# Kernel tuning notes

Measured on AMD Instinct MI355X. Metric: run time of the kernel, lower is better.

The kernel has to match this reference:

```python
import jax, jax.numpy as jnp
import numpy as np

D_MODEL = 1024
NUM_HEADS = 16
D_K = D_MODEL // NUM_HEADS
LN_EPS = 1e-5


def setup_inputs() -> dict:
    key = jax.random.key(0)
    ks = jax.random.split(key, 10)
    s = 1.0 / np.sqrt(D_MODEL)
    x = jax.random.normal(ks[0], (4, 2048, D_MODEL), dtype=jnp.float32)
    Wq = jax.random.uniform(ks[1], (D_MODEL, D_MODEL), jnp.float32, -s, s)
    bq = jax.random.uniform(ks[2], (D_MODEL,), jnp.float32, -s, s)
    Wk = jax.random.uniform(ks[3], (D_MODEL, D_MODEL), jnp.float32, -s, s)
    bk = jax.random.uniform(ks[4], (D_MODEL,), jnp.float32, -s, s)
    Wv = jax.random.uniform(ks[5], (D_MODEL, D_MODEL), jnp.float32, -s, s)
    bv = jax.random.uniform(ks[6], (D_MODEL,), jnp.float32, -s, s)
    Wo = jax.random.uniform(ks[7], (D_MODEL, D_MODEL), jnp.float32, -s, s)
    bo = jax.random.uniform(ks[8], (D_MODEL,), jnp.float32, -s, s)
    gamma = jnp.ones((D_MODEL,), jnp.float32)
    beta = jnp.zeros((D_MODEL,), jnp.float32)
    return {"x": x, "Wq": Wq, "bq": bq, "Wk": Wk, "bk": bk, "Wv": Wv,
            "bv": bv, "Wo": Wo, "bo": bo, "gamma": gamma, "beta": beta}


def reference(x, Wq, bq, Wk, bk, Wv, bv, Wo, bo, gamma, beta):
    B, S, D = x.shape
    H, dk = NUM_HEADS, D_K
    # torch Linear: y = x @ W.T + b
    def proj(W, b):
        y = jnp.einsum('bsd,ed->bse', x, W) + b
        return y.reshape(B, S, H, dk).transpose(0, 2, 1, 3)  # [B,H,S,dk]
    Q = proj(Wq, bq)
    K = proj(Wk, bk)
    V = proj(Wv, bv)
    scores = jnp.einsum('bhqd,bhkd->bhqk', Q, K) / np.sqrt(dk)
    attn = jax.nn.softmax(scores, axis=-1)
    head = jnp.einsum('bhqk,bhkd->bhqd', attn, V)
    head = head.transpose(0, 2, 1, 3).reshape(B, S, D)
    out = jnp.einsum('bsd,ed->bse', head, Wo) + bo
    # LayerNorm
    mu = jnp.mean(out, axis=-1, keepdims=True)
    var = jnp.var(out, axis=-1, keepdims=True)
    out = (out - mu) * jax.lax.rsqrt(var + LN_EPS) * gamma + beta
    # dropout is identity in eval mode
    return x + out
```

## Files before the change

### kernel.cpp

```cpp
#include <hip/hip_runtime.h>
#include <stdint.h>

typedef unsigned short u16;
typedef unsigned int u32;
typedef __attribute__((ext_vector_type(8))) short short8;
typedef __attribute__((ext_vector_type(4))) short short4b;
typedef __attribute__((ext_vector_type(4))) float f32x4;
typedef __attribute__((ext_vector_type(4))) unsigned short u16x4;

#define DEV static __device__ __forceinline__

DEV float bf2f(u16 b) { return __uint_as_float(((uint32_t)b) << 16); }
DEV u16 f2bf(float f) {
  uint32_t u = __float_as_uint(f);
  u += 0x7FFFu + ((u >> 16) & 1u);
  return (u16)(u >> 16);
}
DEV void gld16(const u16* gsrc, u16* ldsdst) {
  __builtin_amdgcn_global_load_lds((const __attribute__((address_space(1))) void*)gsrc,
                                   (__attribute__((address_space(3))) void*)ldsdst, 16, 0, 0);
}
#define MFMA16(a, b, c) __builtin_amdgcn_mfma_f32_16x16x32_bf16(a, b, c, 0, 0, 0)

#define WAITVM4() asm volatile("s_waitcnt vmcnt(4)" ::: "memory")
#define WAITVM0() asm volatile("s_waitcnt vmcnt(0)" ::: "memory")
DEV void barrier() {
  asm volatile("" ::: "memory");
  __builtin_amdgcn_s_barrier();
  asm volatile("" ::: "memory");
}

#if __has_builtin(__builtin_amdgcn_mfma_f32_16x16x16bf16_1k)
DEV f32x4 mfma_k16(short4b a, short4b b, f32x4 c) {
  return __builtin_amdgcn_mfma_f32_16x16x16bf16_1k(a, b, c, 0, 0, 0);
}
#else
DEV f32x4 mfma_k16(short4b a, short4b b, f32x4 c) {
  f32x4 d;
  asm volatile("v_mfma_f32_16x16x16_bf16 %0, %1, %2, %3"
               : "=&v"(d) : "v"(a), "v"(b), "v"(c));
  return d;
}
#endif

#if __has_builtin(__builtin_amdgcn_exp2f)
DEV float fexp2(float x) { return __builtin_amdgcn_exp2f(x); }
#else
DEV float fexp2(float x) { return exp2f(x); }
#endif

DEV u32 cvtpk(float lo, float hi) {
  u32 r;
  asm("v_cvt_pk_bf16_f32 %0, %1, %2" : "=v"(r) : "v"(lo), "v"(hi));
  return r;
}

DEV f32x4 v4max(f32x4 a, f32x4 b) {
  f32x4 r;
  r.x = fmaxf(a.x, b.x); r.y = fmaxf(a.y, b.y);
  r.z = fmaxf(a.z, b.z); r.w = fmaxf(a.w, b.w);
  return r;
}

__global__ __launch_bounds__(256) void k_convert(
    const float* __restrict__ x, const float* __restrict__ wq, const float* __restrict__ wk,
    const float* __restrict__ wv, const float* __restrict__ wo, u16* __restrict__ ws)
{
  int bid = blockIdx.x, t = threadIdx.x;
  const float* src; u16* dst; size_t off;
  if (bid < 8192) { src = x; dst = ws; off = (size_t)bid * 1024; }
  else {
    int r = bid - 8192; int sel = r >> 10; int lb = r & 1023;
    src = sel == 0 ? wq : sel == 1 ? wk : sel == 2 ? wv : wo;
    dst = ws + 8388608u + (size_t)sel * 1048576u;
    off = (size_t)lb * 1024;
  }
  size_t e = off + (size_t)t * 4;
  f32x4 v = *(const f32x4*)(src + e);
  u16x4 o;
  o.x = f2bf(v.x); o.y = f2bf(v.y); o.z = f2bf(v.z); o.w = f2bf(v.w);
  *(u16x4*)(dst + e) = o;
}

DEV void gemm_mainloop(const u16* __restrict__ A, const u16* __restrict__ B,
                       int m0, int n0, u16 (*As)[128 * 32], u16 (*Bs)[128 * 32],
                       f32x4 acc[4][4])
{
  const int tid = threadIdx.x, lane = tid & 63, w = tid >> 6;
  const int fr = lane & 15, g = lane >> 4;
  const int wm = w >> 1, wn = w & 1;

  const int rowA0 = (w * 2 + 0) * 16 + (lane >> 2);
  const int rowA1 = (w * 2 + 1) * 16 + (lane >> 2);
  const int ci = lane & 3;
  const u16* ga0 = A + (size_t)(m0 + rowA0) * 1024 + ((ci ^ (rowA0 & 3)) << 3);
  const u16* ga1 = A + (size_t)(m0 + rowA1) * 1024 + ((ci ^ (rowA1 & 3)) << 3);
  const u16* gb0 = B + (size_t)(n0 + rowA0) * 1024 + ((ci ^ (rowA0 & 3)) << 3);
  const u16* gb1 = B + (size_t)(n0 + rowA1) * 1024 + ((ci ^ (rowA1 & 3)) << 3);
  const int lo0 = (w * 2 + 0) * 512, lo1 = (w * 2 + 1) * 512;

  int raf[4], rbf[4];
#pragma unroll
  for (int i = 0; i < 4; ++i) {
    int rA = wm * 64 + i * 16 + fr;
    raf[i] = rA * 32 + ((g ^ (rA & 3)) << 3);
    int rB = wn * 64 + i * 16 + fr;
    rbf[i] = rB * 32 + ((g ^ (rB & 3)) << 3);
  }

  gld16(ga0, As[0] + lo0);
  gld16(ga1, As[0] + lo1);
  gld16(gb0, Bs[0] + lo0);
  gld16(gb1, Bs[0] + lo1);

  for (int t = 0; t < 32; ++t) {
    const int cur = t & 1;
    if (t < 31) {
      const int k1 = (t + 1) * 32;
      gld16(ga0 + k1, As[cur ^ 1] + lo0);
      gld16(ga1 + k1, As[cur ^ 1] + lo1);
      gld16(gb0 + k1, Bs[cur ^ 1] + lo0);
      gld16(gb1 + k1, Bs[cur ^ 1] + lo1);
      WAITVM4();
    } else {
      WAITVM0();
    }
    barrier();
    const u16* Ab = As[cur];
    short8 af[4], bf[4];
#pragma unroll
    for (int i = 0; i < 4; ++i) af[i] = *(const short8*)&Ab[raf[i]];
#pragma unroll
    for (int i = 0; i < 4; ++i) bf[i] = *(const short8*)&Bs[cur][rbf[i]];
#pragma unroll
    for (int mi = 0; mi < 4; ++mi)
#pragma unroll
      for (int ni = 0; ni < 4; ++ni)
        acc[mi][ni] = MFMA16(af[mi], bf[ni], acc[mi][ni]);
    barrier();
  }
}

__global__ __launch_bounds__(256) void k_gemm_qkv(
    const u16* __restrict__ xb, const u16* __restrict__ wqb, const u16* __restrict__ wkb,
    const u16* __restrict__ wvb, const float* __restrict__ bq, const float* __restrict__ bk,
    const float* __restrict__ bv, u16* __restrict__ Qg, u16* __restrict__ Kg,
    u16* __restrict__ Vtg)
{
  __shared__ u16 As[2][128 * 32], Bs[2][128 * 32];
  const int mb = blockIdx.x, nb_all = blockIdx.y;
  const int mat = nb_all >> 3, nb = nb_all & 7;
  const u16* W = mat == 0 ? wqb : (mat == 1 ? wkb : wvb);
  const float* bias = mat == 0 ? bq : (mat == 1 ? bk : bv);
  const int m0 = mb * 128, n0 = nb * 128;

  f32x4 acc[4][4];
  f32x4 z = {0.f, 0.f, 0.f, 0.f};
#pragma unroll
  for (int i = 0; i < 4; ++i)
#pragma unroll
    for (int j = 0; j < 4; ++j) acc[i][j] = z;

  gemm_mainloop(xb, W, m0, n0, As, Bs, acc);

  const int tid = threadIdx.x, lane = tid & 63, w = tid >> 6;
  const int fr = lane & 15, g = lane >> 4;
  const int wm = w >> 1, wn = w & 1;

  if (mat <= 1) {
    u16* Og = mat == 0 ? Qg : Kg;
    const float scale = mat == 0 ? 0.18033688011112042f : 1.0f;
#pragma unroll
    for (int mi = 0; mi < 4; ++mi)
#pragma unroll
      for (int ni = 0; ni < 4; ++ni) {
        int n = n0 + wn * 64 + ni * 16 + fr;
        float bv_ = bias[n];
        int h = n >> 6, d = n & 63;
#pragma unroll
        for (int r = 0; r < 4; ++r) {
          int m = m0 + wm * 64 + mi * 16 + 4 * g + r;
          int b = m >> 11, s = m & 2047;
          float v = (acc[mi][ni][r] + bv_) * scale;
          Og[(((size_t)(b * 16 + h)) * 2048 + (size_t)s) * 64 + d] = f2bf(v);
        }
      }
  } else {
#pragma unroll
    for (int mi = 0; mi < 4; ++mi)
#pragma unroll
      for (int ni = 0; ni < 4; ++ni) {
        int n = n0 + wn * 64 + ni * 16 + fr;
        float bv_ = bias[n];
        int h = n >> 6, d = n & 63;
        int mbase = m0 + wm * 64 + mi * 16 + 4 * g;
        int b = mbase >> 11, s0 = mbase & 2047;
        u16x4 pk;
        pk.x = f2bf(acc[mi][ni][0] + bv_);
        pk.y = f2bf(acc[mi][ni][1] + bv_);
        pk.z = f2bf(acc[mi][ni][2] + bv_);
        pk.w = f2bf(acc[mi][ni][3] + bv_);
        *(u16x4*)&Vtg[(((size_t)(b * 16 + h)) * 64 + d) * 2048 + s0] = pk;
      }
  }
}

__global__ __launch_bounds__(512, 1) void k_attn(
    const u16* __restrict__ Qg, const u16* __restrict__ Kg, const u16* __restrict__ Vtg,
    u16* __restrict__ headb)
{
  __shared__ u16 K_lds[2][128 * 64];
  __shared__ u16 V_lds[2][64 * 128];
  const int tid = threadIdx.x, lane = tid & 63, w = tid >> 6;
  const int fr = lane & 15, g = lane >> 4;
  const int swz = ((blockIdx.x & 7) << 6) + (blockIdx.x >> 3);
  const int qb = swz & 7, bh = swz >> 3;
  const u16* Qbase = Qg + (size_t)bh * 2048 * 64;
  const u16* Kbase = Kg + (size_t)bh * 2048 * 64;
  const u16* Vbase = Vtg + (size_t)bh * 64 * 2048;

  const int ck0 = w * 2, ck1 = w * 2 + 1;
  const int krow0 = ck0 * 8 + (lane >> 3), krow1 = ck1 * 8 + (lane >> 3);
  const int kci = lane & 7;
  const u16* gk0 = Kbase + (size_t)krow0 * 64 + ((kci ^ (krow0 & 7)) << 3);
  const u16* gk1 = Kbase + (size_t)krow1 * 64 + ((kci ^ (krow1 & 7)) << 3);
  const int vrow0 = ck0 * 4 + (lane >> 4), vrow1 = ck1 * 4 + (lane >> 4);
  const int vci = lane & 15;
  const u16* gv0 = Vbase + (size_t)vrow0 * 2048 + ((vci ^ (vrow0 & 7)) << 3);
  const u16* gv1 = Vbase + (size_t)vrow1 * 2048 + ((vci ^ (vrow1 & 7)) << 3);

  short8 qf[2][2];
#pragma unroll
  for (int mi = 0; mi < 2; ++mi)
#pragma unroll
    for (int kt = 0; kt < 2; ++kt) {
      int qrow = qb * 256 + w * 32 + mi * 16 + fr;
      qf[mi][kt] = *(const short8*)&Qbase[(size_t)qrow * 64 + kt * 32 + g * 8];
    }

  f32x4 po[2][4];
  f32x4 z = {0.f, 0.f, 0.f, 0.f};
#pragma unroll
  for (int mi = 0; mi < 2; ++mi)
#pragma unroll
    for (int dt = 0; dt < 4; ++dt) po[mi][dt] = z;
  float mrun[2] = {-1e30f, -1e30f};
  float lrun[2] = {0.f, 0.f};

  gld16(gk0, K_lds[0] + ck0 * 512);
  gld16(gk1, K_lds[0] + ck1 * 512);
  gld16(gv0, V_lds[0] + ck0 * 512);
  gld16(gv1, V_lds[0] + ck1 * 512);

  for (int kv = 0; kv < 16; ++kv) {
    const int cur = kv & 1;
    if (kv < 15) {
      const int ko = (kv + 1) * 128 * 64;
      const int vo = (kv + 1) * 128;
      gld16(gk0 + ko, K_lds[cur ^ 1] + ck0 * 512);
      gld16(gk1 + ko, K_lds[cur ^ 1] + ck1 * 512);
      gld16(gv0 + vo, V_lds[cur ^ 1] + ck0 * 512);
      gld16(gv1 + vo, V_lds[cur ^ 1] + ck1 * 512);
      WAITVM4();
    } else {
      WAITVM0();
    }
    barrier();
    const u16* Kc = K_lds[cur];
    const u16* Vc = V_lds[cur];

    f32x4 sc[2][8];
#pragma unroll
    for (int mi = 0; mi < 2; ++mi)
#pragma unroll
      for (int nt = 0; nt < 8; ++nt) sc[mi][nt] = z;
    __builtin_amdgcn_s_setprio(1);
#pragma unroll
    for (int nt = 0; nt < 8; ++nt) {
      int rk = nt * 16 + fr;
#pragma unroll
      for (int kt = 0; kt < 2; ++kt) {
        short8 kb = *(const short8*)&Kc[rk * 64 + (((kt * 4 + g) ^ (rk & 7)) << 3)];
        sc[0][nt] = MFMA16(kb, qf[0][kt], sc[0][nt]);
        sc[1][nt] = MFMA16(kb, qf[1][kt], sc[1][nt]);
      }
    }
    __builtin_amdgcn_s_setprio(0);

    short4b pa[2][8];
#pragma unroll
    for (int mi = 0; mi < 2; ++mi) {
      f32x4 m4 = sc[mi][0];
#pragma unroll
      for (int nt = 1; nt < 8; ++nt) m4 = v4max(m4, sc[mi][nt]);
      float mx = fmaxf(fmaxf(m4.x, m4.y), fmaxf(m4.z, m4.w));
      mx = fmaxf(mx, __shfl_xor(mx, 16, 64));
      mx = fmaxf(mx, __shfl_xor(mx, 32, 64));
      const bool defer = __all(mx - mrun[mi] <= 8.0f);
      const float mnew = defer ? mrun[mi] : mx;
      f32x4 s4 = z;
#pragma unroll
      for (int nt = 0; nt < 8; ++nt) {
        f32x4 p;
        p.x = fexp2(sc[mi][nt].x - mnew);
        p.y = fexp2(sc[mi][nt].y - mnew);
        p.z = fexp2(sc[mi][nt].z - mnew);
        p.w = fexp2(sc[mi][nt].w - mnew);
        sc[mi][nt] = p;
        s4 += p;
      }
      float rs = (s4.x + s4.y) + (s4.z + s4.w);
      rs += __shfl_xor(rs, 16, 64);
      rs += __shfl_xor(rs, 32, 64);
      if (defer) {
        lrun[mi] += rs;
      } else {
        float alpha = fexp2(mrun[mi] - mnew);
        lrun[mi] = lrun[mi] * alpha + rs;
        mrun[mi] = mnew;
        f32x4 al4;
#pragma unroll
        for (int r = 0; r < 4; ++r) al4[r] = __shfl(alpha, 4 * g + r, 64);
#pragma unroll
        for (int dt = 0; dt < 4; ++dt) po[mi][dt] *= al4;
      }
#pragma unroll
      for (int nt = 0; nt < 8; ++nt) {
        union { u32 u[2]; short4b s; } cv;
        cv.u[0] = cvtpk(sc[mi][nt].x, sc[mi][nt].y);
        cv.u[1] = cvtpk(sc[mi][nt].z, sc[mi][nt].w);
        pa[mi][nt] = cv.s;
      }
    }

    __builtin_amdgcn_s_setprio(1);
#pragma unroll
    for (int nt = 0; nt < 8; ++nt) {
#pragma unroll
      for (int dt = 0; dt < 4; ++dt) {
        int d = dt * 16 + fr;
        short4b vb = *(const short4b*)&Vc[d * 128 + ((((nt << 1) | (g >> 1)) ^ (d & 7)) << 3) + ((g & 1) << 2)];
        po[0][dt] = mfma_k16(pa[0][nt], vb, po[0][dt]);
        po[1][dt] = mfma_k16(pa[1][nt], vb, po[1][dt]);
      }
    }
    __builtin_amdgcn_s_setprio(0);
    barrier();
  }

  float linv[2][4];
#pragma unroll
  for (int mi = 0; mi < 2; ++mi)
#pragma unroll
    for (int r = 0; r < 4; ++r)
      linv[mi][r] = 1.0f / __shfl(lrun[mi], 4 * g + r, 64);

  const int b = bh >> 4, h = bh & 15;
#pragma unroll
  for (int mi = 0; mi < 2; ++mi)
#pragma unroll
    for (int dt = 0; dt < 4; ++dt)
#pragma unroll
      for (int r = 0; r < 4; ++r) {
        int srow = qb * 256 + w * 32 + mi * 16 + 4 * g + r;
        float v = po[mi][dt][r] * linv[mi][r];
        int e = h * 64 + dt * 16 + fr;
        headb[((size_t)(b * 2048 + srow)) * 1024 + e] = f2bf(v);
      }
}

__global__ __launch_bounds__(256) void k_gemm_o(
    const u16* __restrict__ headb, const u16* __restrict__ wob, const float* __restrict__ bo,
    u16* __restrict__ projb)
{
  __shared__ u16 As[2][128 * 32], Bs[2][128 * 32];
  const int m0 = blockIdx.x * 128, n0 = blockIdx.y * 128;
  f32x4 acc[4][4];
  f32x4 z = {0.f, 0.f, 0.f, 0.f};
#pragma unroll
  for (int i = 0; i < 4; ++i)
#pragma unroll
    for (int j = 0; j < 4; ++j) acc[i][j] = z;

  gemm_mainloop(headb, wob, m0, n0, As, Bs, acc);

  const int tid = threadIdx.x, lane = tid & 63, w = tid >> 6;
  const int fr = lane & 15, g = lane >> 4;
  const int wm = w >> 1, wn = w & 1;
#pragma unroll
  for (int mi = 0; mi < 4; ++mi)
#pragma unroll
    for (int ni = 0; ni < 4; ++ni) {
      int n = n0 + wn * 64 + ni * 16 + fr;
      float bv_ = bo[n];
#pragma unroll
      for (int r = 0; r < 4; ++r) {
        int m = m0 + wm * 64 + mi * 16 + 4 * g + r;
        projb[(size_t)m * 1024 + n] = f2bf(acc[mi][ni][r] + bv_);
      }
    }
}

__global__ __launch_bounds__(256) void k_ln(
    const u16* __restrict__ projb, const float* __restrict__ x,
    const float* __restrict__ gamma, const float* __restrict__ beta, float* __restrict__ out)
{
  __shared__ float sh1[4], sh2[4];
  const int row = blockIdx.x, t = threadIdx.x, lane = t & 63, w = t >> 6;
  const size_t base = (size_t)row * 1024;
  u16x4 pv = *(const u16x4*)&projb[base + t * 4];
  float v0 = bf2f(pv.x), v1 = bf2f(pv.y), v2 = bf2f(pv.z), v3 = bf2f(pv.w);
  float s1 = v0 + v1 + v2 + v3;
  float s2 = v0 * v0 + v1 * v1 + v2 * v2 + v3 * v3;
  for (int m = 1; m < 64; m <<= 1) {
    s1 += __shfl_xor(s1, m, 64);
    s2 += __shfl_xor(s2, m, 64);
  }
  if (lane == 0) { sh1[w] = s1; sh2[w] = s2; }
  __syncthreads();
  s1 = sh1[0] + sh1[1] + sh1[2] + sh1[3];
  s2 = sh2[0] + sh2[1] + sh2[2] + sh2[3];
  float mu = s1 * (1.0f / 1024.0f);
  float var = s2 * (1.0f / 1024.0f) - mu * mu;
  float rsd = rsqrtf(var + 1e-5f);
  f32x4 xv = *(const f32x4*)&x[base + t * 4];
  f32x4 res;
  int e = t * 4;
  res.x = xv.x + (v0 - mu) * rsd * gamma[e + 0] + beta[e + 0];
  res.y = xv.y + (v1 - mu) * rsd * gamma[e + 1] + beta[e + 1];
  res.z = xv.z + (v2 - mu) * rsd * gamma[e + 2] + beta[e + 2];
  res.w = xv.w + (v3 - mu) * rsd * gamma[e + 3] + beta[e + 3];
  *(f32x4*)&out[base + t * 4] = res;
}

extern "C" void kernel_launch(void* const* d_in, const int* in_sizes, int n_in,
                              void* d_out, int out_size, void* d_ws, size_t ws_size,
                              hipStream_t stream)
{
  const float* x     = (const float*)d_in[0];
  const float* Wq    = (const float*)d_in[1];
  const float* bq    = (const float*)d_in[2];
  const float* Wk    = (const float*)d_in[3];
  const float* bk    = (const float*)d_in[4];
  const float* Wv    = (const float*)d_in[5];
  const float* bv    = (const float*)d_in[6];
  const float* Wo    = (const float*)d_in[7];
  const float* bo    = (const float*)d_in[8];
  const float* gamma = (const float*)d_in[9];
  const float* beta  = (const float*)d_in[10];
  float* out = (float*)d_out;

  u16* ws   = (u16*)d_ws;
  u16* xb   = ws;
  u16* wqb  = ws + 8388608;
  u16* wkb  = wqb + 1048576;
  u16* wvb  = wkb + 1048576;
  u16* wob  = wvb + 1048576;
  u16* Qg   = wob + 1048576;
  u16* Kg   = Qg + 8388608;
  u16* Vtg  = Kg + 8388608;
  u16* headb = Vtg + 8388608;
  u16* projb = Qg;

  k_convert<<<12288, 256, 0, stream>>>(x, Wq, Wk, Wv, Wo, ws);
  k_gemm_qkv<<<dim3(64, 24), 256, 0, stream>>>(xb, wqb, wkb, wvb, bq, bk, bv, Qg, Kg, Vtg);
  k_attn<<<dim3(512), 512, 0, stream>>>(Qg, Kg, Vtg, headb);
  k_gemm_o<<<dim3(64, 8), 256, 0, stream>>>(headb, wob, bo, projb);
  k_ln<<<8192, 256, 0, stream>>>(projb, x, gamma, beta, out);
}
```

Before: 256.5 us.

## Replace double-buffered GEMM LDS pipeline with single-buffer load-sync-compute loop

The shared GEMM main loop (used by the QKV and output projections) drops its two-stage LDS ping-pong. It no longer prefetches the next K tile with global_load_lds while MFMAs run on the current one. Each iteration now syncs, loads the tile, syncs again and computes. This halves per-block LDS use from 32KB to 16KB, which may let more blocks share a CU. The cost is that global-memory latency is no longer hidden behind compute within a block.

```diff
diff --git a/kernel.cpp b/kernel.cpp
--- a/kernel.cpp
+++ b/kernel.cpp
@@ -83,8 +83,7 @@
 }
 
 DEV void gemm_mainloop(const u16* __restrict__ A, const u16* __restrict__ B,
-                       int m0, int n0, u16 (*As)[128 * 32], u16 (*Bs)[128 * 32],
-                       f32x4 acc[4][4])
+                       int m0, int n0, u16* As, u16* Bs, f32x4 acc[4][4])
 {
   const int tid = threadIdx.x, lane = tid & 63, w = tid >> 6;
   const int fr = lane & 15, g = lane >> 4;
@@ -97,7 +96,10 @@
   const u16* ga1 = A + (size_t)(m0 + rowA1) * 1024 + ((ci ^ (rowA1 & 3)) << 3);
   const u16* gb0 = B + (size_t)(n0 + rowA0) * 1024 + ((ci ^ (rowA0 & 3)) << 3);
   const u16* gb1 = B + (size_t)(n0 + rowA1) * 1024 + ((ci ^ (rowA1 & 3)) << 3);
-  const int lo0 = (w * 2 + 0) * 512, lo1 = (w * 2 + 1) * 512;
+  u16* lA0 = As + (w * 2 + 0) * 512;
+  u16* lA1 = As + (w * 2 + 1) * 512;
+  u16* lB0 = Bs + (w * 2 + 0) * 512;
+  u16* lB1 = Bs + (w * 2 + 1) * 512;
 
   int raf[4], rbf[4];
 #pragma unroll
@@ -108,36 +110,23 @@
     rbf[i] = rB * 32 + ((g ^ (rB & 3)) << 3);
   }
 
-  gld16(ga0, As[0] + lo0);
-  gld16(ga1, As[0] + lo1);
-  gld16(gb0, Bs[0] + lo0);
-  gld16(gb1, Bs[0] + lo1);
-
-  for (int t = 0; t < 32; ++t) {
-    const int cur = t & 1;
-    if (t < 31) {
-      const int k1 = (t + 1) * 32;
-      gld16(ga0 + k1, As[cur ^ 1] + lo0);
-      gld16(ga1 + k1, As[cur ^ 1] + lo1);
-      gld16(gb0 + k1, Bs[cur ^ 1] + lo0);
-      gld16(gb1 + k1, Bs[cur ^ 1] + lo1);
-      WAITVM4();
-    } else {
-      WAITVM0();
-    }
-    barrier();
-    const u16* Ab = As[cur];
+  for (int k0 = 0; k0 < 1024; k0 += 32) {
+    __syncthreads();
+    gld16(ga0 + k0, lA0);
+    gld16(ga1 + k0, lA1);
+    gld16(gb0 + k0, lB0);
+    gld16(gb1 + k0, lB1);
+    __syncthreads();
     short8 af[4], bf[4];
 #pragma unroll
-    for (int i = 0; i < 4; ++i) af[i] = *(const short8*)&Ab[raf[i]];
-#pragma unroll
-    for (int i = 0; i < 4; ++i) bf[i] = *(const short8*)&Bs[cur][rbf[i]];
+    for (int i = 0; i < 4; ++i) af[i] = *(const short8*)&As[raf[i]];
+#pragma unroll
+    for (int i = 0; i < 4; ++i) bf[i] = *(const short8*)&Bs[rbf[i]];
 #pragma unroll
     for (int mi = 0; mi < 4; ++mi)
 #pragma unroll
       for (int ni = 0; ni < 4; ++ni)
         acc[mi][ni] = MFMA16(af[mi], bf[ni], acc[mi][ni]);
-    barrier();
   }
 }
 
@@ -147,7 +136,7 @@
     const float* __restrict__ bv, u16* __restrict__ Qg, u16* __restrict__ Kg,
     u16* __restrict__ Vtg)
 {
-  __shared__ u16 As[2][128 * 32], Bs[2][128 * 32];
+  __shared__ u16 As[128 * 32], Bs[128 * 32];
   const int mb = blockIdx.x, nb_all = blockIdx.y;
   const int mat = nb_all >> 3, nb = nb_all & 7;
   const u16* W = mat == 0 ? wqb : (mat == 1 ? wkb : wvb);
@@ -373,7 +362,7 @@
     const u16* __restrict__ headb, const u16* __restrict__ wob, const float* __restrict__ bo,
     u16* __restrict__ projb)
 {
-  __shared__ u16 As[2][128 * 32], Bs[2][128 * 32];
+  __shared__ u16 As[128 * 32], Bs[128 * 32];
   const int m0 = blockIdx.x * 128, n0 = blockIdx.y * 128;
   f32x4 acc[4][4];
   f32x4 z = {0.f, 0.f, 0.f, 0.f};
```

After: 241.7 us. 5.8% less time.
